# Performance work log

Measured on AMD Instinct MI355X. Metric: run time of the kernel, lower is better.

Reference implementation:

```python
import jax, jax.numpy as jnp
import numpy as np

N_NODES = 50000
N_EDGES = 300000
N_GRAPHS = 2048
N_FEATS = 128
DIM_OUT = 32


def setup_inputs() -> dict:
    key = jax.random.key(0)
    ks = jax.random.split(key, 10)
    def glorot(k, shape):
        fan_in, fan_out = shape
        lim = (6.0 / (fan_in + fan_out)) ** 0.5
        return jax.random.uniform(k, shape, jnp.float32, -lim, lim)
    x = jax.random.normal(ks[0], (N_NODES, N_FEATS), jnp.float32)
    edge_index = jax.random.randint(ks[1], (2, N_EDGES), 0, N_NODES, jnp.int64)
    batch = jnp.sort(jax.random.randint(ks[2], (N_NODES,), 0, N_GRAPHS, jnp.int64))
    return {
        "x": x,
        "edge_index": edge_index,
        "batch": batch,
        "W1": glorot(ks[3], (N_FEATS, 256)), "b1": jnp.zeros((256,), jnp.float32),
        "W2": glorot(ks[4], (256, 256)),     "b2": jnp.zeros((256,), jnp.float32),
        "W3": glorot(ks[5], (256, 256)),     "b3": jnp.zeros((256,), jnp.float32),
        "Wf1": glorot(ks[6], (256, 128)),    "bf1": jnp.zeros((128,), jnp.float32),
        "Wf2": glorot(ks[7], (128, DIM_OUT)), "bf2": jnp.zeros((DIM_OUT,), jnp.float32),
    }


def _gcn_norm(edge_index, num_nodes):
    # PyG GCNConv default: add self-loops, symmetric D^-1/2 (A+I) D^-1/2 norm.
    loop = jnp.arange(num_nodes, dtype=edge_index.dtype)
    src = jnp.concatenate([edge_index[0], loop])
    dst = jnp.concatenate([edge_index[1], loop])
    deg = jax.ops.segment_sum(jnp.ones_like(dst, jnp.float32), dst, num_segments=num_nodes)
    dinv = jnp.where(deg > 0, deg ** -0.5, 0.0)
    norm = dinv[src] * dinv[dst]  # [E + N]
    return src, dst, norm


def _gcn_conv(x, src, dst, norm, W, b):
    h = x @ W                                # [N, C] transform first (efficient)
    msg = h[src] * norm[:, None]             # gather + scale, [E+N, C]
    agg = jax.ops.segment_sum(msg, dst, num_segments=x.shape[0])
    return agg + b


def reference(x, edge_index, batch, W1, b1, W2, b2, W3, b3, Wf1, bf1, Wf2, bf2):
    n = x.shape[0]
    src, dst, norm = _gcn_norm(edge_index, n)
    h = jax.nn.relu(_gcn_conv(x, src, dst, norm, W1, b1))
    h = jax.nn.relu(_gcn_conv(h, src, dst, norm, W2, b2))
    h = jax.nn.relu(_gcn_conv(h, src, dst, norm, W3, b3))
    # global_mean_pool over batch segment ids
    sums = jax.ops.segment_sum(h, batch, num_segments=N_GRAPHS)
    cnts = jax.ops.segment_sum(jnp.ones((n,), jnp.float32), batch, num_segments=N_GRAPHS)
    hg = sums / jnp.maximum(cnts, 1.0)[:, None]
    h = jax.nn.relu(hg @ Wf1 + bf1)
    return h @ Wf2 + bf2  # [N_GRAPHS, DIM_OUT]
```

## Files before the change

kernel.cpp:

```cpp
#include <hip/hip_runtime.h>
#include <hip/hip_bf16.h>

#define NNODES 50000
#define NEDGES 300000
#define NGRAPH 2048
#define NFEAT  128
#define NHID   256
#define DOUT   32
#define NROWS  50048

typedef __bf16 bf16x8 __attribute__((ext_vector_type(8)));
typedef float  f32x4  __attribute__((ext_vector_type(4)));
typedef unsigned short ushort8v __attribute__((ext_vector_type(8)));
typedef __attribute__((address_space(1))) const void* gas_ptr;
typedef __attribute__((address_space(3))) void* las_ptr;

__device__ __forceinline__ float bf2f(unsigned short u) {
    return __uint_as_float(((unsigned)u) << 16);
}
__device__ __forceinline__ unsigned short f2bf(float f) {
    unsigned u = __float_as_uint(f);
    unsigned r = u + 0x7FFFu + ((u >> 16) & 1u);
    return (unsigned short)(r >> 16);
}
__device__ __forceinline__ float sb2f(unsigned v, int k) {
    return (float)((signed char)(v >> (8 * k)));
}


__global__ __launch_bounds__(256) void prep_k(const float* __restrict__ x, unsigned short* __restrict__ x16,
                                              const float* __restrict__ W1, const float* __restrict__ W2,
                                              const float* __restrict__ W3, const float* __restrict__ Wf1,
                                              const float* __restrict__ Wf2,
                                              unsigned short* __restrict__ Wt1, unsigned short* __restrict__ Wt2,
                                              unsigned short* __restrict__ Wt3, unsigned short* __restrict__ Wf1t,
                                              unsigned short* __restrict__ Wf2t,
                                              int* __restrict__ cnt, int* __restrict__ fill,
                                              int4* __restrict__ adj8z) {
    int idx = blockIdx.x * 256 + threadIdx.x;
    if (idx < 800000) {
        int i = idx * 8;
        float4 a = *(const float4*)&x[i];
        float4 b = *(const float4*)&x[i + 4];
        ushort8v o = { f2bf(a.x), f2bf(a.y), f2bf(a.z), f2bf(a.w),
                       f2bf(b.x), f2bf(b.y), f2bf(b.z), f2bf(b.w) };
        int row = idx >> 4, ch = idx & 15;
        ((ushort8v*)x16)[(size_t)(row << 4) | (ch ^ (row & 7))] = o;
        return;
    }
    int t = idx - 800000;
    if (t < 200704) {
        const float* W; unsigned short* Wt; int K, N, base; bool sw;
        if      (t <  32768) { W = W1;  Wt = Wt1;  K = 128; N = 256; base = 0;      sw = true; }
        else if (t <  98304) { W = W2;  Wt = Wt2;  K = 256; N = 256; base = 32768;  sw = true; }
        else if (t < 163840) { W = W3;  Wt = Wt3;  K = 256; N = 256; base = 98304;  sw = true; }
        else if (t < 196608) { W = Wf1; Wt = Wf1t; K = 256; N = 128; base = 163840; sw = false; }
        else                 { W = Wf2; Wt = Wf2t; K = 128; N = 32;  base = 196608; sw = false; }
        int i = t - base; int n = i / K, k = i - n * K;
        unsigned short v = f2bf(W[(size_t)k * N + n]);
        if (sw) Wt[(k >> 5) * 8192 + n * 32 + (k & 31)] = v;
        else    Wt[i] = v;
        return;
    }
    t -= 200704;
    if (t < NNODES) { cnt[t] = 0; fill[t] = 0; return; }
    t -= NNODES;
    if (t < 200000) { int4 z4 = {0, 0, 0, 0}; adj8z[t] = z4; }
}

__global__ __launch_bounds__(256) void edge_hist_k(const int* __restrict__ dst, int* cnt, int E) {
    int e = blockIdx.x * 256 + threadIdx.x;
    if (e < E) atomicAdd(&cnt[dst[e]], 1);
}

__global__ __launch_bounds__(1024) void scan_block_k(const int* __restrict__ cnt, int* __restrict__ rowp,
                                                     int* __restrict__ part, float* __restrict__ dinv,
                                                     int2* __restrict__ hdr, int n) {
    __shared__ int s[1024];
    int tid = threadIdx.x;
    int i = blockIdx.x * 1024 + tid;
    int v = (i < n) ? cnt[i] : 0;
    if (i < n) {
        float dv = rsqrtf((float)(v + 1));
        dinv[i] = dv;
        hdr[i] = make_int2(v, __float_as_int(dv * dv));
    }
    s[tid] = v;
    __syncthreads();
    for (int off = 1; off < 1024; off <<= 1) {
        int t = (tid >= off) ? s[tid - off] : 0;
        __syncthreads();
        s[tid] += t;
        __syncthreads();
    }
    if (i < n) rowp[i] = s[tid] - v;
    if (tid == 1023) part[blockIdx.x] = s[1023];
}

__global__ __launch_bounds__(256) void scatter_k(const int* __restrict__ src, const int* __restrict__ dst,
                                                 const int* __restrict__ rowp_pre, const int* __restrict__ part,
                                                 int* fill, const float* __restrict__ dinv,
                                                 int2* __restrict__ adj8, int2* __restrict__ adj,
                                                 int* __restrict__ rowp_fin,
                                                 const int* __restrict__ batch, int* __restrict__ gstart,
                                                 int E, int n, int nb) {
    __shared__ int s[64];
    int tid = threadIdx.x;
    if (tid < 64) s[tid] = (tid < nb) ? part[tid] : 0;
    __syncthreads();
    for (int off = 1; off < 64; off <<= 1) {
        int t = 0;
        if (tid < 64 && tid >= off) t = s[tid - off];
        __syncthreads();
        if (tid < 64) s[tid] += t;
        __syncthreads();
    }
    int gid = blockIdx.x * 256 + tid;
    if (gid <= n) {
        if (gid < n) {
            int ch = gid >> 10;
            int base = (ch == 0) ? 0 : s[ch - 1];
            rowp_fin[gid] = rowp_pre[gid] + base;
        } else {
            rowp_fin[n] = s[nb - 1];
        }
    }
    if (gid < n) {
        int b = batch[gid];
        int prev = (gid == 0) ? -1 : batch[gid - 1];
        for (int g = prev + 1; g <= b; ++g) gstart[g] = gid;
        if (gid == n - 1)
            for (int g = b + 1; g <= NGRAPH; ++g) gstart[g] = n;
    }
    if (gid < E) {
        int ss = src[gid], d = dst[gid];
        int f = atomicAdd(&fill[d], 1);
        int2 a; a.x = ss; a.y = __float_as_int(dinv[ss] * dinv[d]);
        if (f < 8) {
            adj8[d * 8 + f] = a;
        } else {
            int ch = d >> 10;
            int base = (ch == 0) ? 0 : s[ch - 1];
            adj[rowp_pre[d] + base + f] = a;
        }
    }
}

template<int CH>
__global__ __launch_bounds__(256) void agg_k(const unsigned short* __restrict__ T,
                                             const int4* __restrict__ adj8,
                                             const int2* __restrict__ hdr,
                                             const int* __restrict__ rowf,
                                             const int2* __restrict__ adj,
                                             unsigned short* __restrict__ z, int n) {
    int g  = threadIdx.x / CH;
    int li = threadIdx.x % CH;
    int node = blockIdx.x * (256 / CH) + g;
    if (node >= n) return;
    const ushort8v* tp = (const ushort8v*)T;
    int2 h = hdr[node];
    int deg = h.x;
    float sw = __int_as_float(h.y);
    ushort8v u = tp[(size_t)node * CH + (li ^ (node & 7))];
    int4 s4[4];
#pragma unroll
    for (int j = 0; j < 4; ++j) s4[j] = adj8[node * 4 + j];
    float ac[8];
#pragma unroll
    for (int k = 0; k < 8; ++k) ac[k] = bf2f(u[k]) * sw;
    int c[8]; float w[8];
#pragma unroll
    for (int j = 0; j < 4; ++j) {
        c[2 * j]     = s4[j].x; w[2 * j]     = __int_as_float(s4[j].y);
        c[2 * j + 1] = s4[j].z; w[2 * j + 1] = __int_as_float(s4[j].w);
    }
    ushort8v mm[8];
#pragma unroll
    for (int j = 0; j < 8; ++j) mm[j] = tp[(size_t)c[j] * CH + (li ^ (c[j] & 7))];
#pragma unroll
    for (int j = 0; j < 8; ++j)
#pragma unroll
        for (int k = 0; k < 8; ++k)
            ac[k] += bf2f(mm[j][k]) * w[j];
    if (deg > 8) {
        int e0 = rowf[node], e1 = e0 + deg;
        for (int e = e0 + 8; e < e1; e += 4) {
            int2 a2[4];
#pragma unroll
            for (int j = 0; j < 4; ++j) {
                int ee = e + j;
                a2[j] = (ee < e1) ? adj[ee] : make_int2(0, 0);
            }
            ushort8v m2[4];
#pragma unroll
            for (int j = 0; j < 4; ++j) m2[j] = tp[(size_t)a2[j].x * CH + (li ^ (a2[j].x & 7))];
#pragma unroll
            for (int j = 0; j < 4; ++j)
#pragma unroll
                for (int k = 0; k < 8; ++k)
                    ac[k] += bf2f(m2[j][k]) * __int_as_float(a2[j].y);
        }
    }
    ushort8v o;
#pragma unroll
    for (int k = 0; k < 8; ++k) o[k] = f2bf(ac[k]);
    ((ushort8v*)z)[(size_t)node * CH + (li ^ (node & 7))] = o;
}

__global__ __launch_bounds__(256) void agg_q_k(const unsigned char* __restrict__ Hq,
                                               const float* __restrict__ csc,
                                               const int4* __restrict__ adj8,
                                               const int2* __restrict__ hdr,
                                               const int* __restrict__ rowf,
                                               const int2* __restrict__ adj,
                                               unsigned short* __restrict__ z, int n) {
    int g  = threadIdx.x >> 5;
    int li = threadIdx.x & 31;
    int node = blockIdx.x * 8 + g;
    if (node >= n) return;
    const uint2* qp = (const uint2*)Hq;
    int2 h = hdr[node];
    int deg = h.x;
    float swgt = __int_as_float(h.y) * csc[node];
    uint2 u = qp[(size_t)node * 32 + li];
    int4 s4[4];
#pragma unroll
    for (int j = 0; j < 4; ++j) s4[j] = adj8[node * 4 + j];
    int c[8]; float w[8];
#pragma unroll
    for (int j = 0; j < 4; ++j) {
        c[2 * j]     = s4[j].x; w[2 * j]     = __int_as_float(s4[j].y);
        c[2 * j + 1] = s4[j].z; w[2 * j + 1] = __int_as_float(s4[j].w);
    }
    uint2 mm[8];
#pragma unroll
    for (int j = 0; j < 8; ++j) mm[j] = qp[(size_t)c[j] * 32 + li];
    float ws[8];
#pragma unroll
    for (int j = 0; j < 8; ++j) ws[j] = w[j] * csc[c[j]];
    float ac[8];
#pragma unroll
    for (int k = 0; k < 4; ++k) {
        ac[k]     = sb2f(u.x, k) * swgt;
        ac[k + 4] = sb2f(u.y, k) * swgt;
    }
#pragma unroll
    for (int j = 0; j < 8; ++j)
#pragma unroll
        for (int k = 0; k < 4; ++k) {
            ac[k]     += sb2f(mm[j].x, k) * ws[j];
            ac[k + 4] += sb2f(mm[j].y, k) * ws[j];
        }
    if (deg > 8) {
        int e0 = rowf[node], e1 = e0 + deg;
        for (int e = e0 + 8; e < e1; e += 4) {
            int2 a2[4];
#pragma unroll
            for (int j = 0; j < 4; ++j) {
                int ee = e + j;
                a2[j] = (ee < e1) ? adj[ee] : make_int2(0, 0);
            }
            uint2 m2[4]; float w2[4];
#pragma unroll
            for (int j = 0; j < 4; ++j) m2[j] = qp[(size_t)a2[j].x * 32 + li];
#pragma unroll
            for (int j = 0; j < 4; ++j) w2[j] = __int_as_float(a2[j].y) * csc[a2[j].x];
#pragma unroll
            for (int j = 0; j < 4; ++j)
#pragma unroll
                for (int k = 0; k < 4; ++k) {
                    ac[k]     += sb2f(m2[j].x, k) * w2[j];
                    ac[k + 4] += sb2f(m2[j].y, k) * w2[j];
                }
        }
    }
    ushort8v o;
#pragma unroll
    for (int k = 0; k < 8; ++k) o[k] = f2bf(ac[k]);
    ((ushort8v*)z)[(size_t)node * 32 + (li ^ (node & 7))] = o;
}

template<int K, bool QOUT>
__global__ __launch_bounds__(512, 2) void gemm_k(const unsigned short* __restrict__ A,
                                                 const unsigned short* __restrict__ Bsw,
                                                 const float* __restrict__ bias,
                                                 unsigned short* __restrict__ C,
                                                 unsigned char* __restrict__ Cq,
                                                 float* __restrict__ csc,
                                                 int M, int flags, int ntiles) {
    constexpr int CPR = K / 8;
    constexpr int LP  = (64 * CPR) / 512;
    __shared__ unsigned short At[64 * K];
    __shared__ unsigned short Et[64 * 264];
    const int tid = threadIdx.x;
    const int lane = tid & 63;
    const int wave = tid >> 6;
    const int m = lane & 15, q = lane >> 4;
    const int wr = (wave >> 2) * 32;
    const int wc = (wave & 3) * 64;

    bf16x8 breg[K / 32][4];
#pragma unroll
    for (int kt = 0; kt < K / 32; ++kt)
#pragma unroll
        for (int j = 0; j < 4; ++j)
            breg[kt][j] = *(const bf16x8*)&Bsw[kt * 8192 + (wc + j * 16 + m) * 32 + q * 8];

    for (int t = blockIdx.x; t < ntiles; t += gridDim.x) {
        const size_t cbase = (size_t)t * 64 * CPR;
#pragma unroll
        for (int p = 0; p < LP; ++p) {
            int u = p * 512 + tid;
            __builtin_amdgcn_global_load_lds((gas_ptr)(A + (cbase + u) * 8),
                                             (las_ptr)&At[(p * 512 + wave * 64) * 8], 16, 0, 0);
        }
        __syncthreads();

        f32x4 acc[2][4] = {};
#pragma unroll
        for (int kt = 0; kt < K / 32; ++kt) {
            bf16x8 af[2];
#pragma unroll
            for (int i = 0; i < 2; ++i) {
                int lr = wr + i * 16 + m;
                af[i] = *(const bf16x8*)&At[(lr * CPR + ((kt * 4 + q) ^ (lr & 7))) * 8];
            }
#pragma unroll
            for (int i = 0; i < 2; ++i)
#pragma unroll
                for (int j = 0; j < 4; ++j)
                    acc[i][j] = __builtin_amdgcn_mfma_f32_16x16x32_bf16(af[i], breg[kt][j], acc[i][j], 0, 0, 0);
        }

#pragma unroll
        for (int i = 0; i < 2; ++i) {
#pragma unroll
            for (int j = 0; j < 4; ++j) {
                int c = wc + j * 16 + m;
                float bv = (flags & 2) ? bias[c] : 0.f;
#pragma unroll
                for (int r = 0; r < 4; ++r) {
                    float v = acc[i][j][r] + bv;
                    if (flags & 1) v = fmaxf(v, 0.f);
                    Et[(wr + i * 16 + q * 4 + r) * 264 + c] = f2bf(v);
                }
            }
        }
        __syncthreads();

        if (QOUT) {
            int row = tid >> 3, ch8 = tid & 7;
            int rr = t * 64 + row;
            ushort8v e[4];
#pragma unroll
            for (int k2 = 0; k2 < 4; ++k2)
                e[k2] = *(const ushort8v*)&Et[row * 264 + ch8 * 32 + k2 * 8];
            float mx = 0.f;
#pragma unroll
            for (int k2 = 0; k2 < 4; ++k2)
#pragma unroll
                for (int k = 0; k < 8; ++k) mx = fmaxf(mx, fabsf(bf2f(e[k2][k])));
            mx = fmaxf(mx, __shfl_xor(mx, 1, 64));
            mx = fmaxf(mx, __shfl_xor(mx, 2, 64));
            mx = fmaxf(mx, __shfl_xor(mx, 4, 64));
            float inv = (mx > 0.f) ? 127.f / mx : 0.f;
            unsigned pk[8];
#pragma unroll
            for (int w2 = 0; w2 < 8; ++w2) {
                unsigned p = 0;
#pragma unroll
                for (int b = 0; b < 4; ++b) {
                    int e8 = w2 * 4 + b;
                    float v = bf2f(e[e8 >> 3][e8 & 7]);
                    int qv = (int)rintf(v * inv);
                    p |= ((unsigned)(qv & 255)) << (8 * b);
                }
                pk[w2] = p;
            }
            if (rr < M) {
                uint4* dst = (uint4*)&Cq[(size_t)rr * 256 + ch8 * 32];
                dst[0] = make_uint4(pk[0], pk[1], pk[2], pk[3]);
                dst[1] = make_uint4(pk[4], pk[5], pk[6], pk[7]);
                if (ch8 == 0) csc[rr] = mx * (1.f / 127.f);
            }
        } else {
#pragma unroll
            for (int u0 = 0; u0 < 4; ++u0) {
                int u = u0 * 512 + tid;
                int row = u >> 5, cc = u & 31;
                int rr = t * 64 + row;
                if (rr < M)
                    ((ushort8v*)C)[(size_t)rr * 32 + (cc ^ (rr & 7))] = *(const ushort8v*)&Et[row * 264 + cc * 8];
            }
        }
    }
}

__global__ __launch_bounds__(256) void pool_k(const unsigned short* __restrict__ h,
                                              const int* __restrict__ gstart,
                                              unsigned short* __restrict__ hg) {
    __shared__ float red[4][256];
    int g = blockIdx.x;
    int wave = threadIdx.x >> 6, lane = threadIdx.x & 63;
    int s = gstart[g], e = gstart[g + 1];
    int ch = lane >> 1, sub = lane & 1;
    const ushort4* hp = (const ushort4*)h;
    float4 acc = make_float4(0.f, 0.f, 0.f, 0.f);
    for (int i = s + wave; i < e; i += 4) {
        ushort4 v = hp[((size_t)i * 32 + (ch ^ (i & 7))) * 2 + sub];
        acc.x += bf2f(v.x); acc.y += bf2f(v.y); acc.z += bf2f(v.z); acc.w += bf2f(v.w);
    }
    *(float4*)&red[wave][lane * 4] = acc;
    __syncthreads();
    if (wave == 0) {
        float inv = 1.f / fmaxf((float)(e - s), 1.f);
        float v0 = red[0][lane*4+0] + red[1][lane*4+0] + red[2][lane*4+0] + red[3][lane*4+0];
        float v1 = red[0][lane*4+1] + red[1][lane*4+1] + red[2][lane*4+1] + red[3][lane*4+1];
        float v2 = red[0][lane*4+2] + red[1][lane*4+2] + red[2][lane*4+2] + red[3][lane*4+2];
        float v3 = red[0][lane*4+3] + red[1][lane*4+3] + red[2][lane*4+3] + red[3][lane*4+3];
        ushort4 o = { f2bf(v0 * inv), f2bf(v1 * inv), f2bf(v2 * inv), f2bf(v3 * inv) };
        ((ushort4*)(hg + (size_t)g * NHID))[lane] = o;
    }
}

__global__ __launch_bounds__(256) void mlp_head_k(const unsigned short* __restrict__ HG,
                                                  const unsigned short* __restrict__ Wf1t,
                                                  const unsigned short* __restrict__ Wf2t,
                                                  const float* __restrict__ bf1, const float* __restrict__ bf2,
                                                  float* __restrict__ out) {
    __shared__ unsigned short As1[128 * 32];
    __shared__ unsigned short Bs1[128 * 32];
    __shared__ unsigned short R[128 * 128];
    __shared__ unsigned short Bs2[32 * 128];
    const int tid = threadIdx.x;
    const int lane = tid & 63, wave = tid >> 6;
    const int m = lane & 15, q = lane >> 4;
    const int rowBase = blockIdx.x * 128;
    const int wr = (wave >> 1) * 64;
    const int wc = (wave & 1) * 64;

#pragma unroll
    for (int c2 = 0; c2 < 2; ++c2) {
        const unsigned short* g = &Wf2t[(c2 * 256 + tid) * 8];
        __builtin_amdgcn_global_load_lds((gas_ptr)g, (las_ptr)&Bs2[(c2 * 256 + wave * 64) * 8], 16, 0, 0);
    }

    f32x4 acc[4][4] = {};
    for (int kt = 0; kt < 256; kt += 32) {
#pragma unroll
        for (int c2 = 0; c2 < 2; ++c2) {
            int u = c2 * 256 + tid;
            int row = u >> 2, kp = u & 3;
            const unsigned short* ga = &HG[(size_t)(rowBase + row) * 256 + kt + kp * 8];
            const unsigned short* gb = &Wf1t[(size_t)row * 256 + kt + kp * 8];
            __builtin_amdgcn_global_load_lds((gas_ptr)ga, (las_ptr)&As1[(c2 * 256 + wave * 64) * 8], 16, 0, 0);
            __builtin_amdgcn_global_load_lds((gas_ptr)gb, (las_ptr)&Bs1[(c2 * 256 + wave * 64) * 8], 16, 0, 0);
        }
        __syncthreads();
        bf16x8 af[4], bfr[4];
#pragma unroll
        for (int i = 0; i < 4; ++i) af[i] = *(const bf16x8*)&As1[(wr + i * 16 + m) * 32 + q * 8];
#pragma unroll
        for (int j = 0; j < 4; ++j) bfr[j] = *(const bf16x8*)&Bs1[(wc + j * 16 + m) * 32 + q * 8];
#pragma unroll
        for (int i = 0; i < 4; ++i)
#pragma unroll
            for (int j = 0; j < 4; ++j)
                acc[i][j] = __builtin_amdgcn_mfma_f32_16x16x32_bf16(af[i], bfr[j], acc[i][j], 0, 0, 0);
        __syncthreads();
    }
#pragma unroll
    for (int i = 0; i < 4; ++i)
#pragma unroll
        for (int j = 0; j < 4; ++j) {
            int c = wc + j * 16 + m;
            float bv = bf1[c];
#pragma unroll
            for (int r = 0; r < 4; ++r) {
                int rr = wr + i * 16 + q * 4 + r;
                R[rr * 128 + c] = f2bf(fmaxf(acc[i][j][r] + bv, 0.f));
            }
        }
    __syncthreads();

    const int wr2 = wave * 32;
    f32x4 acc2[2][2] = {};
#pragma unroll
    for (int s2 = 0; s2 < 4; ++s2) {
        bf16x8 af2[2], bf22[2];
#pragma unroll
        for (int i = 0; i < 2; ++i) af2[i] = *(const bf16x8*)&R[(wr2 + i * 16 + m) * 128 + s2 * 32 + q * 8];
#pragma unroll
        for (int ct = 0; ct < 2; ++ct) bf22[ct] = *(const bf16x8*)&Bs2[(ct * 16 + m) * 128 + s2 * 32 + q * 8];
#pragma unroll
        for (int i = 0; i < 2; ++i)
#pragma unroll
            for (int ct = 0; ct < 2; ++ct)
                acc2[i][ct] = __builtin_amdgcn_mfma_f32_16x16x32_bf16(af2[i], bf22[ct], acc2[i][ct], 0, 0, 0);
    }
#pragma unroll
    for (int i = 0; i < 2; ++i)
#pragma unroll
        for (int ct = 0; ct < 2; ++ct) {
            int c = ct * 16 + m;
            float bv = bf2[c];
#pragma unroll
            for (int r = 0; r < 4; ++r) {
                int rr = rowBase + wr2 + i * 16 + q * 4 + r;
                out[(size_t)rr * 32 + c] = acc2[i][ct][r] + bv;
            }
        }
}

extern "C" void kernel_launch(void* const* d_in, const int* in_sizes, int n_in,
                              void* d_out, int out_size, void* d_ws, size_t ws_size,
                              hipStream_t stream) {
    const float* x    = (const float*)d_in[0];
    const int*   ei   = (const int*)d_in[1];
    const int*   batch= (const int*)d_in[2];
    const float* W1   = (const float*)d_in[3];
    const float* b1   = (const float*)d_in[4];
    const float* W2   = (const float*)d_in[5];
    const float* b2   = (const float*)d_in[6];
    const float* W3   = (const float*)d_in[7];
    const float* b3   = (const float*)d_in[8];
    const float* Wf1  = (const float*)d_in[9];
    const float* bf1  = (const float*)d_in[10];
    const float* Wf2  = (const float*)d_in[11];
    const float* bf2  = (const float*)d_in[12];
    float* out = (float*)d_out;

    const int* e_src = ei;
    const int* e_dst = ei + NEDGES;

    char* ws = (char*)d_ws;
    size_t off = 0;
    auto alloc = [&](size_t bytes) -> void* {
        void* p = (void*)(ws + off);
        off += (bytes + 255) & ~(size_t)255;
        return p;
    };
    unsigned short* X16 = (unsigned short*)alloc((size_t)NROWS * NFEAT * 2);
    unsigned short* Za  = (unsigned short*)alloc((size_t)NROWS * NFEAT * 2);
    unsigned short* Zb  = (unsigned short*)alloc((size_t)NROWS * NHID * 2);
    unsigned short* Ha  = (unsigned short*)alloc((size_t)NROWS * NHID * 2);
    unsigned char*  Hq  = (unsigned char*)alloc((size_t)NROWS * NHID);
    float*          csc = (float*)alloc((size_t)NROWS * 4);
    unsigned short* Wt1 = (unsigned short*)alloc((size_t)NHID * NFEAT * 2);
    unsigned short* Wt2 = (unsigned short*)alloc((size_t)NHID * NHID * 2);
    unsigned short* Wt3 = (unsigned short*)alloc((size_t)NHID * NHID * 2);
    unsigned short* Wf1t= (unsigned short*)alloc((size_t)NFEAT * NHID * 2);
    unsigned short* Wf2t= (unsigned short*)alloc((size_t)DOUT * NFEAT * 2);
    unsigned short* HG  = (unsigned short*)alloc((size_t)NGRAPH * NHID * 2);
    float* dinv = (float*)alloc((size_t)NNODES * 4);
    int*   cnt  = (int*)alloc((size_t)NNODES * 4);
    int*   fill = (int*)alloc((size_t)NNODES * 4);
    int*   rowp = (int*)alloc((size_t)(NNODES + 1) * 4);
    int*   rowf = (int*)alloc((size_t)(NNODES + 1) * 4);
    int2*  adj8 = (int2*)alloc((size_t)NNODES * 8 * 8);
    int2*  adj  = (int2*)alloc((size_t)NEDGES * 8);
    int2*  hdr  = (int2*)alloc((size_t)NNODES * 8);
    int*   part = (int*)alloc((size_t)64 * 4);
    int*   gstart = (int*)alloc((size_t)(NGRAPH + 1) * 4);
    (void)alloc(131072);

    const int nb = (NNODES + 1023) / 1024;

    hipLaunchKernelGGL(prep_k, dim3((1250704 + 255) / 256), dim3(256), 0, stream,
                       x, X16, W1, W2, W3, Wf1, Wf2, Wt1, Wt2, Wt3, Wf1t, Wf2t, cnt, fill,
                       (int4*)adj8);
    hipLaunchKernelGGL(edge_hist_k, dim3((NEDGES + 255) / 256), dim3(256), 0, stream, e_dst, cnt, NEDGES);
    hipLaunchKernelGGL(scan_block_k, dim3(nb), dim3(1024), 0, stream, cnt, rowp, part, dinv, hdr, NNODES);
    hipLaunchKernelGGL(scatter_k, dim3((NEDGES + 255) / 256), dim3(256), 0, stream,
                       e_src, e_dst, rowp, part, fill, dinv, adj8, adj, rowf, batch, gstart,
                       NEDGES, NNODES, nb);

    const int ntiles = NROWS / 64;
    hipLaunchKernelGGL((agg_k<16>), dim3((NNODES + 15) / 16), dim3(256), 0, stream,
                       X16, (const int4*)adj8, hdr, rowf, adj, Za, NNODES);
    hipLaunchKernelGGL((gemm_k<128, true>), dim3(512), dim3(512), 0, stream,
                       Za, Wt1, b1, (unsigned short*)nullptr, Hq, csc, NNODES, 3, ntiles);
    hipLaunchKernelGGL(agg_q_k, dim3((NNODES + 7) / 8), dim3(256), 0, stream,
                       Hq, csc, (const int4*)adj8, hdr, rowf, adj, Zb, NNODES);
    hipLaunchKernelGGL((gemm_k<256, true>), dim3(512), dim3(512), 0, stream,
                       Zb, Wt2, b2, (unsigned short*)nullptr, Hq, csc, NNODES, 3, ntiles);
    hipLaunchKernelGGL(agg_q_k, dim3((NNODES + 7) / 8), dim3(256), 0, stream,
                       Hq, csc, (const int4*)adj8, hdr, rowf, adj, Zb, NNODES);
    hipLaunchKernelGGL((gemm_k<256, false>), dim3(512), dim3(512), 0, stream,
                       Zb, Wt3, b3, Ha, Hq, csc, NNODES, 3, ntiles);

    hipLaunchKernelGGL(pool_k, dim3(NGRAPH), dim3(256), 0, stream, Ha, gstart, HG);

    hipLaunchKernelGGL(mlp_head_k, dim3(NGRAPH / 128), dim3(256), 0, stream,
                       HG, Wf1t, Wf2t, bf1, bf2, out);
}
```

Measured before the change: 268.3 us.

## Fuse mean-pool into last GEMM epilogue and widen agg_q per-thread loads

The final GCN GEMM no longer writes the bf16 hidden matrix. It accumulates per-graph column sums into a float buffer with run-length-compressed atomics over sorted batch ids, and the head kernel applies 1/count while loading. This removes the Ha write/read and the pool kernel launch, at the cost of global float atomics and an extra zeroing pass in prep. Separately, agg_q_k now uses 16 lanes per node with 16-byte int8 gathers instead of 32 lanes with 8-byte gathers, halving load instructions per neighbour but doubling register accumulators.

```diff
diff --git a/kernel.cpp b/kernel.cpp
--- a/kernel.cpp
+++ b/kernel.cpp
@@ -36,7 +36,7 @@
                                               unsigned short* __restrict__ Wt3, unsigned short* __restrict__ Wf1t,
                                               unsigned short* __restrict__ Wf2t,
                                               int* __restrict__ cnt, int* __restrict__ fill,
-                                              int4* __restrict__ adj8z) {
+                                              int4* __restrict__ adj8z, float4* __restrict__ hgz) {
     int idx = blockIdx.x * 256 + threadIdx.x;
     if (idx < 800000) {
         int i = idx * 8;
@@ -65,7 +65,9 @@
     t -= 200704;
     if (t < NNODES) { cnt[t] = 0; fill[t] = 0; return; }
     t -= NNODES;
-    if (t < 200000) { int4 z4 = {0, 0, 0, 0}; adj8z[t] = z4; }
+    if (t < 200000) { int4 z4 = {0, 0, 0, 0}; adj8z[t] = z4; return; }
+    t -= 200000;
+    if (t < 131072) { hgz[t] = make_float4(0.f, 0.f, 0.f, 0.f); }
 }
 
 __global__ __launch_bounds__(256) void edge_hist_k(const int* __restrict__ dst, int* cnt, int E) {
@@ -214,15 +216,15 @@
                                                const int* __restrict__ rowf,
                                                const int2* __restrict__ adj,
                                                unsigned short* __restrict__ z, int n) {
-    int g  = threadIdx.x >> 5;
-    int li = threadIdx.x & 31;
-    int node = blockIdx.x * 8 + g;
+    int g  = threadIdx.x >> 4;
+    int li = threadIdx.x & 15;
+    int node = blockIdx.x * 16 + g;
     if (node >= n) return;
-    const uint2* qp = (const uint2*)Hq;
+    const uint4* qp = (const uint4*)Hq;
     int2 h = hdr[node];
     int deg = h.x;
     float swgt = __int_as_float(h.y) * csc[node];
-    uint2 u = qp[(size_t)node * 32 + li];
+    uint4 u = qp[(size_t)node * 16 + li];
     int4 s4[4];
 #pragma unroll
     for (int j = 0; j < 4; ++j) s4[j] = adj8[node * 4 + j];
@@ -232,24 +234,28 @@
         c[2 * j]     = s4[j].x; w[2 * j]     = __int_as_float(s4[j].y);
         c[2 * j + 1] = s4[j].z; w[2 * j + 1] = __int_as_float(s4[j].w);
     }
-    uint2 mm[8];
-#pragma unroll
-    for (int j = 0; j < 8; ++j) mm[j] = qp[(size_t)c[j] * 32 + li];
+    uint4 mm[8];
+#pragma unroll
+    for (int j = 0; j < 8; ++j) mm[j] = qp[(size_t)c[j] * 16 + li];
     float ws[8];
 #pragma unroll
     for (int j = 0; j < 8; ++j) ws[j] = w[j] * csc[c[j]];
-    float ac[8];
+    float ac[16];
 #pragma unroll
     for (int k = 0; k < 4; ++k) {
-        ac[k]     = sb2f(u.x, k) * swgt;
-        ac[k + 4] = sb2f(u.y, k) * swgt;
+        ac[k]      = sb2f(u.x, k) * swgt;
+        ac[k + 4]  = sb2f(u.y, k) * swgt;
+        ac[k + 8]  = sb2f(u.z, k) * swgt;
+        ac[k + 12] = sb2f(u.w, k) * swgt;
     }
 #pragma unroll
     for (int j = 0; j < 8; ++j)
 #pragma unroll
         for (int k = 0; k < 4; ++k) {
-            ac[k]     += sb2f(mm[j].x, k) * ws[j];
-            ac[k + 4] += sb2f(mm[j].y, k) * ws[j];
+            ac[k]      += sb2f(mm[j].x, k) * ws[j];
+            ac[k + 4]  += sb2f(mm[j].y, k) * ws[j];
+            ac[k + 8]  += sb2f(mm[j].z, k) * ws[j];
+            ac[k + 12] += sb2f(mm[j].w, k) * ws[j];
         }
     if (deg > 8) {
         int e0 = rowf[node], e1 = e0 + deg;
@@ -260,38 +266,44 @@
                 int ee = e + j;
                 a2[j] = (ee < e1) ? adj[ee] : make_int2(0, 0);
             }
-            uint2 m2[4]; float w2[4];
-#pragma unroll
-            for (int j = 0; j < 4; ++j) m2[j] = qp[(size_t)a2[j].x * 32 + li];
+            uint4 m2[4]; float w2[4];
+#pragma unroll
+            for (int j = 0; j < 4; ++j) m2[j] = qp[(size_t)a2[j].x * 16 + li];
 #pragma unroll
             for (int j = 0; j < 4; ++j) w2[j] = __int_as_float(a2[j].y) * csc[a2[j].x];
 #pragma unroll
             for (int j = 0; j < 4; ++j)
 #pragma unroll
                 for (int k = 0; k < 4; ++k) {
-                    ac[k]     += sb2f(m2[j].x, k) * w2[j];
-                    ac[k + 4] += sb2f(m2[j].y, k) * w2[j];
+                    ac[k]      += sb2f(m2[j].x, k) * w2[j];
+                    ac[k + 4]  += sb2f(m2[j].y, k) * w2[j];
+                    ac[k + 8]  += sb2f(m2[j].z, k) * w2[j];
+                    ac[k + 12] += sb2f(m2[j].w, k) * w2[j];
                 }
         }
     }
-    ushort8v o;
-#pragma unroll
-    for (int k = 0; k < 8; ++k) o[k] = f2bf(ac[k]);
-    ((ushort8v*)z)[(size_t)node * 32 + (li ^ (node & 7))] = o;
-}
-
-template<int K, bool QOUT>
+    ushort8v o0, o1;
+#pragma unroll
+    for (int k = 0; k < 8; ++k) { o0[k] = f2bf(ac[k]); o1[k] = f2bf(ac[k + 8]); }
+    size_t base = (size_t)node * 32;
+    ((ushort8v*)z)[base + ((2 * li)     ^ (node & 7))] = o0;
+    ((ushort8v*)z)[base + ((2 * li + 1) ^ (node & 7))] = o1;
+}
+
+template<int K, int MODE>
 __global__ __launch_bounds__(512, 2) void gemm_k(const unsigned short* __restrict__ A,
                                                  const unsigned short* __restrict__ Bsw,
                                                  const float* __restrict__ bias,
-                                                 unsigned short* __restrict__ C,
                                                  unsigned char* __restrict__ Cq,
                                                  float* __restrict__ csc,
+                                                 float* __restrict__ HGacc,
+                                                 const int* __restrict__ batch,
                                                  int M, int flags, int ntiles) {
     constexpr int CPR = K / 8;
     constexpr int LP  = (64 * CPR) / 512;
     __shared__ unsigned short At[64 * K];
     __shared__ unsigned short Et[64 * 264];
+    __shared__ int sbatch[64];
     const int tid = threadIdx.x;
     const int lane = tid & 63;
     const int wave = tid >> 6;
@@ -346,9 +358,13 @@
                 }
             }
         }
-        __syncthreads();
-
-        if (QOUT) {
+        if (MODE == 2 && tid < 64) {
+            int rr = t * 64 + tid;
+            sbatch[tid] = (rr < M) ? batch[rr] : -1;
+        }
+        __syncthreads();
+
+        if (MODE == 1) {
             int row = tid >> 3, ch8 = tid & 7;
             int rr = t * 64 + row;
             ushort8v e[4];
@@ -384,46 +400,25 @@
                 if (ch8 == 0) csc[rr] = mx * (1.f / 127.f);
             }
         } else {
-#pragma unroll
-            for (int u0 = 0; u0 < 4; ++u0) {
-                int u = u0 * 512 + tid;
-                int row = u >> 5, cc = u & 31;
-                int rr = t * 64 + row;
-                if (rr < M)
-                    ((ushort8v*)C)[(size_t)rr * 32 + (cc ^ (rr & 7))] = *(const ushort8v*)&Et[row * 264 + cc * 8];
-            }
-        }
-    }
-}
-
-__global__ __launch_bounds__(256) void pool_k(const unsigned short* __restrict__ h,
-                                              const int* __restrict__ gstart,
-                                              unsigned short* __restrict__ hg) {
-    __shared__ float red[4][256];
-    int g = blockIdx.x;
-    int wave = threadIdx.x >> 6, lane = threadIdx.x & 63;
-    int s = gstart[g], e = gstart[g + 1];
-    int ch = lane >> 1, sub = lane & 1;
-    const ushort4* hp = (const ushort4*)h;
-    float4 acc = make_float4(0.f, 0.f, 0.f, 0.f);
-    for (int i = s + wave; i < e; i += 4) {
-        ushort4 v = hp[((size_t)i * 32 + (ch ^ (i & 7))) * 2 + sub];
-        acc.x += bf2f(v.x); acc.y += bf2f(v.y); acc.z += bf2f(v.z); acc.w += bf2f(v.w);
-    }
-    *(float4*)&red[wave][lane * 4] = acc;
-    __syncthreads();
-    if (wave == 0) {
-        float inv = 1.f / fmaxf((float)(e - s), 1.f);
-        float v0 = red[0][lane*4+0] + red[1][lane*4+0] + red[2][lane*4+0] + red[3][lane*4+0];
-        float v1 = red[0][lane*4+1] + red[1][lane*4+1] + red[2][lane*4+1] + red[3][lane*4+1];
-        float v2 = red[0][lane*4+2] + red[1][lane*4+2] + red[2][lane*4+2] + red[3][lane*4+2];
-        float v3 = red[0][lane*4+3] + red[1][lane*4+3] + red[2][lane*4+3] + red[3][lane*4+3];
-        ushort4 o = { f2bf(v0 * inv), f2bf(v1 * inv), f2bf(v2 * inv), f2bf(v3 * inv) };
-        ((ushort4*)(hg + (size_t)g * NHID))[lane] = o;
-    }
-}
-
-__global__ __launch_bounds__(256) void mlp_head_k(const unsigned short* __restrict__ HG,
+            int c = tid & 255, hh = tid >> 8;
+            int gcur = sbatch[hh * 32];
+            float acp = 0.f;
+#pragma unroll 1
+            for (int r = 0; r < 32; ++r) {
+                int gb = sbatch[hh * 32 + r];
+                if (gb != gcur) {
+                    if (gcur >= 0) atomicAdd(&HGacc[(size_t)gcur * 256 + c], acp);
+                    acp = 0.f; gcur = gb;
+                }
+                if (gb >= 0) acp += bf2f(Et[(hh * 32 + r) * 264 + c]);
+            }
+            if (gcur >= 0) atomicAdd(&HGacc[(size_t)gcur * 256 + c], acp);
+        }
+    }
+}
+
+__global__ __launch_bounds__(256) void mlp_head_k(const float* __restrict__ HGacc,
+                                                  const int* __restrict__ gstart,
                                                   const unsigned short* __restrict__ Wf1t,
                                                   const unsigned short* __restrict__ Wf2t,
                                                   const float* __restrict__ bf1, const float* __restrict__ bf2,
@@ -432,6 +427,7 @@
     __shared__ unsigned short Bs1[128 * 32];
     __shared__ unsigned short R[128 * 128];
     __shared__ unsigned short Bs2[32 * 128];
+    __shared__ float invc[128];
     const int tid = threadIdx.x;
     const int lane = tid & 63, wave = tid >> 6;
     const int m = lane & 15, q = lane >> 4;
@@ -444,16 +440,31 @@
         const unsigned short* g = &Wf2t[(c2 * 256 + tid) * 8];
         __builtin_amdgcn_global_load_lds((gas_ptr)g, (las_ptr)&Bs2[(c2 * 256 + wave * 64) * 8], 16, 0, 0);
     }
+    if (tid < 128) {
+        int g0 = rowBase + tid;
+        invc[tid] = 1.f / fmaxf((float)(gstart[g0 + 1] - gstart[g0]), 1.f);
+    }
+    __syncthreads();
 
     f32x4 acc[4][4] = {};
     for (int kt = 0; kt < 256; kt += 32) {
+        {
+            int row = tid >> 1, half = tid & 1;
+            const float4* src = (const float4*)&HGacc[(size_t)(rowBase + row) * 256 + kt + half * 16];
+            float4 f0 = src[0], f1 = src[1], f2 = src[2], f3 = src[3];
+            float sc = invc[row];
+            ushort8v p0 = { f2bf(f0.x * sc), f2bf(f0.y * sc), f2bf(f0.z * sc), f2bf(f0.w * sc),
+                            f2bf(f1.x * sc), f2bf(f1.y * sc), f2bf(f1.z * sc), f2bf(f1.w * sc) };
+            ushort8v p1 = { f2bf(f2.x * sc), f2bf(f2.y * sc), f2bf(f2.z * sc), f2bf(f2.w * sc),
+                            f2bf(f3.x * sc), f2bf(f3.y * sc), f2bf(f3.z * sc), f2bf(f3.w * sc) };
+            *(ushort8v*)&As1[row * 32 + half * 16] = p0;
+            *(ushort8v*)&As1[row * 32 + half * 16 + 8] = p1;
+        }
 #pragma unroll
         for (int c2 = 0; c2 < 2; ++c2) {
             int u = c2 * 256 + tid;
             int row = u >> 2, kp = u & 3;
-            const unsigned short* ga = &HG[(size_t)(rowBase + row) * 256 + kt + kp * 8];
             const unsigned short* gb = &Wf1t[(size_t)row * 256 + kt + kp * 8];
-            __builtin_amdgcn_global_load_lds((gas_ptr)ga, (las_ptr)&As1[(c2 * 256 + wave * 64) * 8], 16, 0, 0);
             __builtin_amdgcn_global_load_lds((gas_ptr)gb, (las_ptr)&Bs1[(c2 * 256 + wave * 64) * 8], 16, 0, 0);
         }
         __syncthreads();
@@ -543,15 +554,14 @@
     unsigned short* X16 = (unsigned short*)alloc((size_t)NROWS * NFEAT * 2);
     unsigned short* Za  = (unsigned short*)alloc((size_t)NROWS * NFEAT * 2);
     unsigned short* Zb  = (unsigned short*)alloc((size_t)NROWS * NHID * 2);
-    unsigned short* Ha  = (unsigned short*)alloc((size_t)NROWS * NHID * 2);
     unsigned char*  Hq  = (unsigned char*)alloc((size_t)NROWS * NHID);
     float*          csc = (float*)alloc((size_t)NROWS * 4);
+    float*          HGacc = (float*)alloc((size_t)NGRAPH * NHID * 4);
     unsigned short* Wt1 = (unsigned short*)alloc((size_t)NHID * NFEAT * 2);
     unsigned short* Wt2 = (unsigned short*)alloc((size_t)NHID * NHID * 2);
     unsigned short* Wt3 = (unsigned short*)alloc((size_t)NHID * NHID * 2);
     unsigned short* Wf1t= (unsigned short*)alloc((size_t)NFEAT * NHID * 2);
     unsigned short* Wf2t= (unsigned short*)alloc((size_t)DOUT * NFEAT * 2);
-    unsigned short* HG  = (unsigned short*)alloc((size_t)NGRAPH * NHID * 2);
     float* dinv = (float*)alloc((size_t)NNODES * 4);
     int*   cnt  = (int*)alloc((size_t)NNODES * 4);
     int*   fill = (int*)alloc((size_t)NNODES * 4);
@@ -566,9 +576,9 @@
 
     const int nb = (NNODES + 1023) / 1024;
 
-    hipLaunchKernelGGL(prep_k, dim3((1250704 + 255) / 256), dim3(256), 0, stream,
+    hipLaunchKernelGGL(prep_k, dim3((1381776 + 255) / 256), dim3(256), 0, stream,
                        x, X16, W1, W2, W3, Wf1, Wf2, Wt1, Wt2, Wt3, Wf1t, Wf2t, cnt, fill,
-                       (int4*)adj8);
+                       (int4*)adj8, (float4*)HGacc);
     hipLaunchKernelGGL(edge_hist_k, dim3((NEDGES + 255) / 256), dim3(256), 0, stream, e_dst, cnt, NEDGES);
     hipLaunchKernelGGL(scan_block_k, dim3(nb), dim3(1024), 0, stream, cnt, rowp, part, dinv, hdr, NNODES);
     hipLaunchKernelGGL(scatter_k, dim3((NEDGES + 255) / 256), dim3(256), 0, stream,
@@ -578,19 +588,17 @@
     const int ntiles = NROWS / 64;
     hipLaunchKernelGGL((agg_k<16>), dim3((NNODES + 15) / 16), dim3(256), 0, stream,
                        X16, (const int4*)adj8, hdr, rowf, adj, Za, NNODES);
-    hipLaunchKernelGGL((gemm_k<128, true>), dim3(512), dim3(512), 0, stream,
-                       Za, Wt1, b1, (unsigned short*)nullptr, Hq, csc, NNODES, 3, ntiles);
-    hipLaunchKernelGGL(agg_q_k, dim3((NNODES + 7) / 8), dim3(256), 0, stream,
+    hipLaunchKernelGGL((gemm_k<128, 1>), dim3(512), dim3(512), 0, stream,
+                       Za, Wt1, b1, Hq, csc, (float*)nullptr, (const int*)nullptr, NNODES, 3, ntiles);
+    hipLaunchKernelGGL(agg_q_k, dim3((NNODES + 15) / 16), dim3(256), 0, stream,
                        Hq, csc, (const int4*)adj8, hdr, rowf, adj, Zb, NNODES);
-    hipLaunchKernelGGL((gemm_k<256, true>), dim3(512), dim3(512), 0, stream,
-                       Zb, Wt2, b2, (unsigned short*)nullptr, Hq, csc, NNODES, 3, ntiles);
-    hipLaunchKernelGGL(agg_q_k, dim3((NNODES + 7) / 8), dim3(256), 0, stream,
+    hipLaunchKernelGGL((gemm_k<256, 1>), dim3(512), dim3(512), 0, stream,
+                       Zb, Wt2, b2, Hq, csc, (float*)nullptr, (const int*)nullptr, NNODES, 3, ntiles);
+    hipLaunchKernelGGL(agg_q_k, dim3((NNODES + 15) / 16), dim3(256), 0, stream,
                        Hq, csc, (const int4*)adj8, hdr, rowf, adj, Zb, NNODES);
-    hipLaunchKernelGGL((gemm_k<256, false>), dim3(512), dim3(512), 0, stream,
-                       Zb, Wt3, b3, Ha, Hq, csc, NNODES, 3, ntiles);
-
-    hipLaunchKernelGGL(pool_k, dim3(NGRAPH), dim3(256), 0, stream, Ha, gstart, HG);
+    hipLaunchKernelGGL((gemm_k<256, 2>), dim3(512), dim3(512), 0, stream,
+                       Zb, Wt3, b3, (unsigned char*)nullptr, (float*)nullptr, HGacc, batch, NNODES, 3, ntiles);
 
     hipLaunchKernelGGL(mlp_head_k, dim3(NGRAPH / 128), dim3(256), 0, stream,
-                       HG, Wf1t, Wf2t, bf1, bf2, out);
-}
+                       HGacc, gstart, Wf1t, Wf2t, bf1, bf2, out);
+}
```

Result: slower. 275.6 us (+2.7%).

## Quantize GCN layer GEMMs to int8 MFMA with per-row and per-column scales

Applied to the files above, without the earlier changes.

Aggregation kernels now write their outputs as int8 with a per-node absmax scale instead of bf16. The three layer weight matrices are quantized per output column to int8 in the prep kernel. The GEMM now runs on i8 MFMA (16x16x64) and dequantizes in the epilogue using both scales. This halves the bytes the aggregation writes and the GEMM reads, and uses the higher int8 MFMA rate, at the cost of extra quantization error in activations and weights.

```diff
diff --git a/kernel.cpp b/kernel.cpp
--- a/kernel.cpp
+++ b/kernel.cpp
@@ -11,6 +11,7 @@
 
 typedef __bf16 bf16x8 __attribute__((ext_vector_type(8)));
 typedef float  f32x4  __attribute__((ext_vector_type(4)));
+typedef int    i32x4  __attribute__((ext_vector_type(4)));
 typedef unsigned short ushort8v __attribute__((ext_vector_type(8)));
 typedef __attribute__((address_space(1))) const void* gas_ptr;
 typedef __attribute__((address_space(3))) void* las_ptr;
@@ -28,13 +29,47 @@
 }
 
 
+template<int K>
+__device__ __forceinline__ void wquant(const float* __restrict__ W, unsigned char* __restrict__ Wq,
+                                       float* __restrict__ bsc, int t) {
+    constexpr int EPR = K / 16;
+    int n = t >> 4, p = t & 15;
+    float vals[EPR];
+    float mx = 0.f;
+#pragma unroll
+    for (int j = 0; j < EPR; ++j) {
+        float v = W[(size_t)(p * EPR + j) * 256 + n];
+        vals[j] = v;
+        mx = fmaxf(mx, fabsf(v));
+    }
+    mx = fmaxf(mx, __shfl_xor(mx, 1, 16));
+    mx = fmaxf(mx, __shfl_xor(mx, 2, 16));
+    mx = fmaxf(mx, __shfl_xor(mx, 4, 16));
+    mx = fmaxf(mx, __shfl_xor(mx, 8, 16));
+    float inv = (mx > 0.f) ? 127.f / mx : 0.f;
+#pragma unroll
+    for (int j4 = 0; j4 < EPR / 4; ++j4) {
+        unsigned pw = 0;
+#pragma unroll
+        for (int b = 0; b < 4; ++b) {
+            int qv = (int)rintf(vals[j4 * 4 + b] * inv);
+            pw |= ((unsigned)(qv & 255)) << (8 * b);
+        }
+        int k = p * EPR + j4 * 4;
+        *(unsigned*)&Wq[(k >> 6) * 16384 + n * 64 + (k & 63)] = pw;
+    }
+    if (p == 0) bsc[n] = mx * (1.f / 127.f);
+}
+
 __global__ __launch_bounds__(256) void prep_k(const float* __restrict__ x, unsigned short* __restrict__ x16,
                                               const float* __restrict__ W1, const float* __restrict__ W2,
                                               const float* __restrict__ W3, const float* __restrict__ Wf1,
                                               const float* __restrict__ Wf2,
-                                              unsigned short* __restrict__ Wt1, unsigned short* __restrict__ Wt2,
-                                              unsigned short* __restrict__ Wt3, unsigned short* __restrict__ Wf1t,
-                                              unsigned short* __restrict__ Wf2t,
+                                              unsigned char* __restrict__ Wq1, unsigned char* __restrict__ Wq2,
+                                              unsigned char* __restrict__ Wq3,
+                                              float* __restrict__ bsc1, float* __restrict__ bsc2,
+                                              float* __restrict__ bsc3,
+                                              unsigned short* __restrict__ Wf1t, unsigned short* __restrict__ Wf2t,
                                               int* __restrict__ cnt, int* __restrict__ fill,
                                               int4* __restrict__ adj8z) {
     int idx = blockIdx.x * 256 + threadIdx.x;
@@ -49,20 +84,21 @@
         return;
     }
     int t = idx - 800000;
-    if (t < 200704) {
-        const float* W; unsigned short* Wt; int K, N, base; bool sw;
-        if      (t <  32768) { W = W1;  Wt = Wt1;  K = 128; N = 256; base = 0;      sw = true; }
-        else if (t <  98304) { W = W2;  Wt = Wt2;  K = 256; N = 256; base = 32768;  sw = true; }
-        else if (t < 163840) { W = W3;  Wt = Wt3;  K = 256; N = 256; base = 98304;  sw = true; }
-        else if (t < 196608) { W = Wf1; Wt = Wf1t; K = 256; N = 128; base = 163840; sw = false; }
-        else                 { W = Wf2; Wt = Wf2t; K = 128; N = 32;  base = 196608; sw = false; }
-        int i = t - base; int n = i / K, k = i - n * K;
-        unsigned short v = f2bf(W[(size_t)k * N + n]);
-        if (sw) Wt[(k >> 5) * 8192 + n * 32 + (k & 31)] = v;
-        else    Wt[i] = v;
+    if (t < 4096)  { wquant<128>(W1, Wq1, bsc1, t); return; }
+    t -= 4096;
+    if (t < 4096)  { wquant<256>(W2, Wq2, bsc2, t); return; }
+    t -= 4096;
+    if (t < 4096)  { wquant<256>(W3, Wq3, bsc3, t); return; }
+    t -= 4096;
+    if (t < 36864) {
+        const float* W; unsigned short* Wt; int K, N;
+        if (t < 32768) { W = Wf1; Wt = Wf1t; K = 256; N = 128; }
+        else           { W = Wf2; Wt = Wf2t; K = 128; N = 32; t -= 32768; }
+        int n = t / K, k = t - n * K;
+        Wt[t] = f2bf(W[(size_t)k * N + n]);
         return;
     }
-    t -= 200704;
+    t -= 36864;
     if (t < NNODES) { cnt[t] = 0; fill[t] = 0; return; }
     t -= NNODES;
     if (t < 200000) { int4 z4 = {0, 0, 0, 0}; adj8z[t] = z4; }
@@ -146,22 +182,22 @@
     }
 }
 
-template<int CH>
-__global__ __launch_bounds__(256) void agg_k(const unsigned short* __restrict__ T,
-                                             const int4* __restrict__ adj8,
-                                             const int2* __restrict__ hdr,
-                                             const int* __restrict__ rowf,
-                                             const int2* __restrict__ adj,
-                                             unsigned short* __restrict__ z, int n) {
-    int g  = threadIdx.x / CH;
-    int li = threadIdx.x % CH;
-    int node = blockIdx.x * (256 / CH) + g;
+__global__ __launch_bounds__(256) void agg1_k(const unsigned short* __restrict__ T,
+                                              const int4* __restrict__ adj8,
+                                              const int2* __restrict__ hdr,
+                                              const int* __restrict__ rowf,
+                                              const int2* __restrict__ adj,
+                                              unsigned char* __restrict__ z8,
+                                              float* __restrict__ asc, int n) {
+    int g  = threadIdx.x >> 4;
+    int li = threadIdx.x & 15;
+    int node = blockIdx.x * 16 + g;
     if (node >= n) return;
     const ushort8v* tp = (const ushort8v*)T;
     int2 h = hdr[node];
     int deg = h.x;
     float sw = __int_as_float(h.y);
-    ushort8v u = tp[(size_t)node * CH + (li ^ (node & 7))];
+    ushort8v u = tp[(size_t)node * 16 + (li ^ (node & 7))];
     int4 s4[4];
 #pragma unroll
     for (int j = 0; j < 4; ++j) s4[j] = adj8[node * 4 + j];
@@ -176,7 +212,7 @@
     }
     ushort8v mm[8];
 #pragma unroll
-    for (int j = 0; j < 8; ++j) mm[j] = tp[(size_t)c[j] * CH + (li ^ (c[j] & 7))];
+    for (int j = 0; j < 8; ++j) mm[j] = tp[(size_t)c[j] * 16 + (li ^ (c[j] & 7))];
 #pragma unroll
     for (int j = 0; j < 8; ++j)
 #pragma unroll
@@ -193,7 +229,7 @@
             }
             ushort8v m2[4];
 #pragma unroll
-            for (int j = 0; j < 4; ++j) m2[j] = tp[(size_t)a2[j].x * CH + (li ^ (a2[j].x & 7))];
+            for (int j = 0; j < 4; ++j) m2[j] = tp[(size_t)a2[j].x * 16 + (li ^ (a2[j].x & 7))];
 #pragma unroll
             for (int j = 0; j < 4; ++j)
 #pragma unroll
@@ -201,10 +237,24 @@
                     ac[k] += bf2f(m2[j][k]) * __int_as_float(a2[j].y);
         }
     }
-    ushort8v o;
-#pragma unroll
-    for (int k = 0; k < 8; ++k) o[k] = f2bf(ac[k]);
-    ((ushort8v*)z)[(size_t)node * CH + (li ^ (node & 7))] = o;
+    float mx = 0.f;
+#pragma unroll
+    for (int k = 0; k < 8; ++k) mx = fmaxf(mx, fabsf(ac[k]));
+    mx = fmaxf(mx, __shfl_xor(mx, 1, 16));
+    mx = fmaxf(mx, __shfl_xor(mx, 2, 16));
+    mx = fmaxf(mx, __shfl_xor(mx, 4, 16));
+    mx = fmaxf(mx, __shfl_xor(mx, 8, 16));
+    float inv = (mx > 0.f) ? 127.f / mx : 0.f;
+    unsigned w0 = 0, w1 = 0;
+#pragma unroll
+    for (int k = 0; k < 4; ++k) {
+        int q0 = (int)rintf(ac[k] * inv);
+        int q1 = (int)rintf(ac[k + 4] * inv);
+        w0 |= ((unsigned)(q0 & 255)) << (8 * k);
+        w1 |= ((unsigned)(q1 & 255)) << (8 * k);
+    }
+    ((uint2*)z8)[(size_t)node * 16 + ((li >> 1) ^ (node & 7)) * 2 + (li & 1)] = make_uint2(w0, w1);
+    if (li == 0) asc[node] = mx * (1.f / 127.f);
 }
 
 __global__ __launch_bounds__(256) void agg_q_k(const unsigned char* __restrict__ Hq,
@@ -213,7 +263,8 @@
                                                const int2* __restrict__ hdr,
                                                const int* __restrict__ rowf,
                                                const int2* __restrict__ adj,
-                                               unsigned short* __restrict__ z, int n) {
+                                               unsigned char* __restrict__ z8,
+                                               float* __restrict__ asc, int n) {
     int g  = threadIdx.x >> 5;
     int li = threadIdx.x & 31;
     int node = blockIdx.x * 8 + g;
@@ -274,24 +325,42 @@
                 }
         }
     }
-    ushort8v o;
-#pragma unroll
-    for (int k = 0; k < 8; ++k) o[k] = f2bf(ac[k]);
-    ((ushort8v*)z)[(size_t)node * 32 + (li ^ (node & 7))] = o;
-}
-
-template<int K, bool QOUT>
-__global__ __launch_bounds__(512, 2) void gemm_k(const unsigned short* __restrict__ A,
-                                                 const unsigned short* __restrict__ Bsw,
+    float mx = 0.f;
+#pragma unroll
+    for (int k = 0; k < 8; ++k) mx = fmaxf(mx, fabsf(ac[k]));
+    mx = fmaxf(mx, __shfl_xor(mx, 1, 32));
+    mx = fmaxf(mx, __shfl_xor(mx, 2, 32));
+    mx = fmaxf(mx, __shfl_xor(mx, 4, 32));
+    mx = fmaxf(mx, __shfl_xor(mx, 8, 32));
+    mx = fmaxf(mx, __shfl_xor(mx, 16, 32));
+    float inv = (mx > 0.f) ? 127.f / mx : 0.f;
+    unsigned w0 = 0, w1 = 0;
+#pragma unroll
+    for (int k = 0; k < 4; ++k) {
+        int q0 = (int)rintf(ac[k] * inv);
+        int q1 = (int)rintf(ac[k + 4] * inv);
+        w0 |= ((unsigned)(q0 & 255)) << (8 * k);
+        w1 |= ((unsigned)(q1 & 255)) << (8 * k);
+    }
+    ((uint2*)z8)[(size_t)node * 32 + ((li >> 1) ^ (node & 7)) * 2 + (li & 1)] = make_uint2(w0, w1);
+    if (li == 0) asc[node] = mx * (1.f / 127.f);
+}
+
+template<int K, int MODE>
+__global__ __launch_bounds__(512, 2) void gemm_k(const unsigned char* __restrict__ A,
+                                                 const unsigned char* __restrict__ Bq,
+                                                 const float* __restrict__ bscale,
+                                                 const float* __restrict__ asc,
                                                  const float* __restrict__ bias,
                                                  unsigned short* __restrict__ C,
                                                  unsigned char* __restrict__ Cq,
                                                  float* __restrict__ csc,
                                                  int M, int flags, int ntiles) {
-    constexpr int CPR = K / 8;
+    constexpr int CPR = K / 16;
     constexpr int LP  = (64 * CPR) / 512;
-    __shared__ unsigned short At[64 * K];
+    __shared__ unsigned char  At[64 * K];
     __shared__ unsigned short Et[64 * 264];
+    __shared__ float sAsc[64];
     const int tid = threadIdx.x;
     const int lane = tid & 63;
     const int wave = tid >> 6;
@@ -299,37 +368,38 @@
     const int wr = (wave >> 2) * 32;
     const int wc = (wave & 3) * 64;
 
-    bf16x8 breg[K / 32][4];
-#pragma unroll
-    for (int kt = 0; kt < K / 32; ++kt)
+    i32x4 breg[K / 64][4];
+#pragma unroll
+    for (int kt = 0; kt < K / 64; ++kt)
 #pragma unroll
         for (int j = 0; j < 4; ++j)
-            breg[kt][j] = *(const bf16x8*)&Bsw[kt * 8192 + (wc + j * 16 + m) * 32 + q * 8];
+            breg[kt][j] = *(const i32x4*)&Bq[kt * 16384 + (wc + j * 16 + m) * 64 + q * 16];
 
     for (int t = blockIdx.x; t < ntiles; t += gridDim.x) {
-        const size_t cbase = (size_t)t * 64 * CPR;
+        const size_t cbase = (size_t)t * 64 * K;
 #pragma unroll
         for (int p = 0; p < LP; ++p) {
             int u = p * 512 + tid;
-            __builtin_amdgcn_global_load_lds((gas_ptr)(A + (cbase + u) * 8),
-                                             (las_ptr)&At[(p * 512 + wave * 64) * 8], 16, 0, 0);
-        }
-        __syncthreads();
-
-        f32x4 acc[2][4] = {};
-#pragma unroll
-        for (int kt = 0; kt < K / 32; ++kt) {
-            bf16x8 af[2];
+            __builtin_amdgcn_global_load_lds((gas_ptr)(A + cbase + (size_t)u * 16),
+                                             (las_ptr)&At[(p * 512 + wave * 64) * 16], 16, 0, 0);
+        }
+        if (tid < 64) sAsc[tid] = asc[t * 64 + tid];
+        __syncthreads();
+
+        i32x4 acc[2][4] = {};
+#pragma unroll
+        for (int kt = 0; kt < K / 64; ++kt) {
+            i32x4 af[2];
 #pragma unroll
             for (int i = 0; i < 2; ++i) {
                 int lr = wr + i * 16 + m;
-                af[i] = *(const bf16x8*)&At[(lr * CPR + ((kt * 4 + q) ^ (lr & 7))) * 8];
+                af[i] = *(const i32x4*)&At[lr * K + (((kt * 4 + q) ^ (lr & 7)) * 16)];
             }
 #pragma unroll
             for (int i = 0; i < 2; ++i)
 #pragma unroll
                 for (int j = 0; j < 4; ++j)
-                    acc[i][j] = __builtin_amdgcn_mfma_f32_16x16x32_bf16(af[i], breg[kt][j], acc[i][j], 0, 0, 0);
+                    acc[i][j] = __builtin_amdgcn_mfma_i32_16x16x64_i8(af[i], breg[kt][j], acc[i][j], 0, 0, 0);
         }
 
 #pragma unroll
@@ -338,17 +408,19 @@
             for (int j = 0; j < 4; ++j) {
                 int c = wc + j * 16 + m;
                 float bv = (flags & 2) ? bias[c] : 0.f;
+                float bs = bscale[c];
 #pragma unroll
                 for (int r = 0; r < 4; ++r) {
-                    float v = acc[i][j][r] + bv;
+                    int row = wr + i * 16 + q * 4 + r;
+                    float v = (float)acc[i][j][r] * (sAsc[row] * bs) + bv;
                     if (flags & 1) v = fmaxf(v, 0.f);
-                    Et[(wr + i * 16 + q * 4 + r) * 264 + c] = f2bf(v);
+                    Et[row * 264 + c] = f2bf(v);
                 }
             }
         }
         __syncthreads();
 
-        if (QOUT) {
+        if (MODE == 1) {
             int row = tid >> 3, ch8 = tid & 7;
             int rr = t * 64 + row;
             ushort8v e[4];
@@ -541,17 +613,21 @@
         return p;
     };
     unsigned short* X16 = (unsigned short*)alloc((size_t)NROWS * NFEAT * 2);
-    unsigned short* Za  = (unsigned short*)alloc((size_t)NROWS * NFEAT * 2);
-    unsigned short* Zb  = (unsigned short*)alloc((size_t)NROWS * NHID * 2);
-    unsigned short* Ha  = (unsigned short*)alloc((size_t)NROWS * NHID * 2);
+    unsigned char*  Za8 = (unsigned char*)alloc((size_t)NROWS * NFEAT);
+    unsigned char*  Zb8 = (unsigned char*)alloc((size_t)NROWS * NHID);
+    float*          asc = (float*)alloc((size_t)NROWS * 4);
     unsigned char*  Hq  = (unsigned char*)alloc((size_t)NROWS * NHID);
     float*          csc = (float*)alloc((size_t)NROWS * 4);
-    unsigned short* Wt1 = (unsigned short*)alloc((size_t)NHID * NFEAT * 2);
-    unsigned short* Wt2 = (unsigned short*)alloc((size_t)NHID * NHID * 2);
-    unsigned short* Wt3 = (unsigned short*)alloc((size_t)NHID * NHID * 2);
+    unsigned short* Ha  = (unsigned short*)alloc((size_t)NROWS * NHID * 2);
+    unsigned short* HG  = (unsigned short*)alloc((size_t)NGRAPH * NHID * 2);
+    unsigned char*  Wq1 = (unsigned char*)alloc((size_t)NFEAT * NHID);
+    unsigned char*  Wq2 = (unsigned char*)alloc((size_t)NHID * NHID);
+    unsigned char*  Wq3 = (unsigned char*)alloc((size_t)NHID * NHID);
+    float*          bsc1= (float*)alloc((size_t)NHID * 4);
+    float*          bsc2= (float*)alloc((size_t)NHID * 4);
+    float*          bsc3= (float*)alloc((size_t)NHID * 4);
     unsigned short* Wf1t= (unsigned short*)alloc((size_t)NFEAT * NHID * 2);
     unsigned short* Wf2t= (unsigned short*)alloc((size_t)DOUT * NFEAT * 2);
-    unsigned short* HG  = (unsigned short*)alloc((size_t)NGRAPH * NHID * 2);
     float* dinv = (float*)alloc((size_t)NNODES * 4);
     int*   cnt  = (int*)alloc((size_t)NNODES * 4);
     int*   fill = (int*)alloc((size_t)NNODES * 4);
@@ -565,10 +641,11 @@
     (void)alloc(131072);
 
     const int nb = (NNODES + 1023) / 1024;
-
-    hipLaunchKernelGGL(prep_k, dim3((1250704 + 255) / 256), dim3(256), 0, stream,
-                       x, X16, W1, W2, W3, Wf1, Wf2, Wt1, Wt2, Wt3, Wf1t, Wf2t, cnt, fill,
-                       (int4*)adj8);
+    const int nprep = 800000 + 4096 * 3 + 36864 + NNODES + 200000;
+
+    hipLaunchKernelGGL(prep_k, dim3((nprep + 255) / 256), dim3(256), 0, stream,
+                       x, X16, W1, W2, W3, Wf1, Wf2, Wq1, Wq2, Wq3, bsc1, bsc2, bsc3,
+                       Wf1t, Wf2t, cnt, fill, (int4*)adj8);
     hipLaunchKernelGGL(edge_hist_k, dim3((NEDGES + 255) / 256), dim3(256), 0, stream, e_dst, cnt, NEDGES);
     hipLaunchKernelGGL(scan_block_k, dim3(nb), dim3(1024), 0, stream, cnt, rowp, part, dinv, hdr, NNODES);
     hipLaunchKernelGGL(scatter_k, dim3((NEDGES + 255) / 256), dim3(256), 0, stream,
@@ -576,18 +653,18 @@
                        NEDGES, NNODES, nb);
 
     const int ntiles = NROWS / 64;
-    hipLaunchKernelGGL((agg_k<16>), dim3((NNODES + 15) / 16), dim3(256), 0, stream,
-                       X16, (const int4*)adj8, hdr, rowf, adj, Za, NNODES);
-    hipLaunchKernelGGL((gemm_k<128, true>), dim3(512), dim3(512), 0, stream,
-                       Za, Wt1, b1, (unsigned short*)nullptr, Hq, csc, NNODES, 3, ntiles);
+    hipLaunchKernelGGL(agg1_k, dim3((NNODES + 15) / 16), dim3(256), 0, stream,
+                       X16, (const int4*)adj8, hdr, rowf, adj, Za8, asc, NNODES);
+    hipLaunchKernelGGL((gemm_k<128, 1>), dim3(512), dim3(512), 0, stream,
+                       Za8, Wq1, bsc1, asc, b1, (unsigned short*)nullptr, Hq, csc, NNODES, 3, ntiles);
     hipLaunchKernelGGL(agg_q_k, dim3((NNODES + 7) / 8), dim3(256), 0, stream,
-                       Hq, csc, (const int4*)adj8, hdr, rowf, adj, Zb, NNODES);
-    hipLaunchKernelGGL((gemm_k<256, true>), dim3(512), dim3(512), 0, stream,
-                       Zb, Wt2, b2, (unsigned short*)nullptr, Hq, csc, NNODES, 3, ntiles);
+                       Hq, csc, (const int4*)adj8, hdr, rowf, adj, Zb8, asc, NNODES);
+    hipLaunchKernelGGL((gemm_k<256, 1>), dim3(512), dim3(512), 0, stream,
+                       Zb8, Wq2, bsc2, asc, b2, (unsigned short*)nullptr, Hq, csc, NNODES, 3, ntiles);
     hipLaunchKernelGGL(agg_q_k, dim3((NNODES + 7) / 8), dim3(256), 0, stream,
-                       Hq, csc, (const int4*)adj8, hdr, rowf, adj, Zb, NNODES);
-    hipLaunchKernelGGL((gemm_k<256, false>), dim3(512), dim3(512), 0, stream,
-                       Zb, Wt3, b3, Ha, Hq, csc, NNODES, 3, ntiles);
+                       Hq, csc, (const int4*)adj8, hdr, rowf, adj, Zb8, asc, NNODES);
+    hipLaunchKernelGGL((gemm_k<256, 0>), dim3(512), dim3(512), 0, stream,
+                       Zb8, Wq3, bsc3, asc, b3, Ha, (unsigned char*)nullptr, (float*)nullptr, NNODES, 3, ntiles);
 
     hipLaunchKernelGGL(pool_k, dim3(NGRAPH), dim3(256), 0, stream, Ha, gstart, HG);
 
```

Result: faster. 252.0 us (-6.1%).
